# Kernel optimization log

Hardware: AMD Instinct MI355X
Metric: run time of the kernel (lower is better)

Reference implementation:

```python
import jax, jax.numpy as jnp
import numpy as np

B, S, D, H = 2, 2048, 2048, 16
HD = D // H  # 128, head_dim (even, as asserted)
MAX_POS = 2048


def setup_inputs() -> dict:
    key = jax.random.key(0)
    ks = jax.random.split(key, 5)
    x = jax.random.normal(ks[0], (B, S, D), jnp.float32)
    Wq = jax.random.normal(ks[1], (D, D), jnp.float32) * 0.02
    Wk = jax.random.normal(ks[2], (D, D), jnp.float32) * 0.02
    Wv = jax.random.normal(ks[3], (D, D), jnp.float32) * 0.02
    Wo = jax.random.normal(ks[4], (D, D), jnp.float32) * 0.02
    # standard RoPE tables: [MAX_POS, HD]
    inv_freq = 1.0 / (10000.0 ** (jnp.arange(0, HD, 2, dtype=jnp.float32) / HD))
    angles = jnp.arange(MAX_POS, dtype=jnp.float32)[:, None] * inv_freq  # [P, HD/2]
    emb = jnp.concatenate([angles, angles], axis=-1)  # [P, HD]
    cos_freqs = jnp.cos(emb)
    sin_freqs = jnp.sin(emb)
    position_ids = jnp.broadcast_to(jnp.arange(S, dtype=jnp.int32), (B, S))
    return {"x": x, "cos_freqs": cos_freqs, "sin_freqs": sin_freqs,
            "Wq": Wq, "Wk": Wk, "Wv": Wv, "Wo": Wo,
            "position_ids": position_ids}


def _apply_rope(t, cos, sin, position_ids):
    # t: [b, s, h, hd]; cos/sin: [P, hd]; position_ids: [b, s]
    c = cos[position_ids][:, :, None, :]  # [b, s, 1, hd]
    s_ = sin[position_ids][:, :, None, :]
    t1, t2 = jnp.split(t, 2, axis=-1)
    rot = jnp.concatenate([-t2, t1], axis=-1)  # rotate-half
    return t * c + rot * s_


def reference(x, cos_freqs, sin_freqs, Wq, Wk, Wv, Wo, position_ids):
    b, s, d = x.shape
    q = (x @ Wq).reshape(b, s, H, HD)
    k = (x @ Wk).reshape(b, s, H, HD)  # n_kv_heads == n_heads
    v = (x @ Wv).reshape(b, s, H, HD)
    q = _apply_rope(q, cos_freqs, sin_freqs, position_ids)
    k = _apply_rope(k, cos_freqs, sin_freqs, position_ids)
    # [b, h, s, hd]
    q_t = jnp.swapaxes(q, 1, 2)
    k_t = jnp.swapaxes(k, 1, 2)
    v_t = jnp.swapaxes(v, 1, 2)
    scale = 1.0 / jnp.sqrt(jnp.float32(HD))
    scores = jnp.einsum('bhsd,bhtd->bhst', q_t, k_t) * scale  # O(s^2) matrix
    causal = jnp.tril(jnp.ones((s, s), dtype=bool))
    scores = jnp.where(causal[None, None, :, :], scores, -1e9)
    weights = jax.nn.softmax(scores, axis=-1)
    out = jnp.einsum('bhst,bhtd->bhsd', weights, v_t)
    out = jnp.swapaxes(out, 1, 2).reshape(b, s, d)
    out = out @ Wo
    return (out, k, v)  # kv_cache is post-RoPE, pre-transpose as in original
```

## Files before the change

### kernel.cpp

```cpp
#include <hip/hip_runtime.h>
#include <hip/hip_bf16.h>

#define B_ 2
#define S_ 2048
#define D_ 2048
#define H_ 16
#define HD_ 128
#define M_ (B_*S_)
#define BSD ((size_t)B_*S_*D_)

typedef short bf16x8 __attribute__((ext_vector_type(8)));
typedef float floatx4 __attribute__((ext_vector_type(4)));
typedef __hip_bfloat16 bf16;

union cv8 { bf16 h[8]; uint4 u; bf16x8 v; };

__device__ inline cv8 cvt8(const float4 a, const float4 b) {
    cv8 c;
    c.h[0] = __float2bfloat16(a.x); c.h[1] = __float2bfloat16(a.y);
    c.h[2] = __float2bfloat16(a.z); c.h[3] = __float2bfloat16(a.w);
    c.h[4] = __float2bfloat16(b.x); c.h[5] = __float2bfloat16(b.y);
    c.h[6] = __float2bfloat16(b.z); c.h[7] = __float2bfloat16(b.w);
    return c;
}

__device__ __forceinline__ void gld16(const void* g, void* l) {
    __builtin_amdgcn_global_load_lds(
        (const __attribute__((address_space(1))) unsigned int*)g,
        (__attribute__((address_space(3))) unsigned int*)l,
        16, 0, 0);
}

__global__ __launch_bounds__(256) void transpose_w(
    const float* __restrict__ W, bf16* __restrict__ Wt, int N, int K)
{
    __shared__ float T[32][33];
    const int k0 = blockIdx.x * 32, n0 = blockIdx.y * 32;
    const int r = threadIdx.x >> 3, c4 = (threadIdx.x & 7) * 4;
    float4 v = *(const float4*)&W[(size_t)(k0 + r) * N + n0 + c4];
    T[r][c4+0] = v.x; T[r][c4+1] = v.y; T[r][c4+2] = v.z; T[r][c4+3] = v.w;
    __syncthreads();
    union { bf16 h[4]; uint2 u; } o;
    #pragma unroll
    for (int i = 0; i < 4; ++i) o.h[i] = __float2bfloat16(T[c4 + i][r]);
    *(uint2*)&Wt[(size_t)(n0 + r) * K + k0 + c4] = o.u;
}

__global__ __launch_bounds__(256) void transpose_w_s(
    const float* __restrict__ W, bf16* __restrict__ Wt, int N, int K)
{
    __shared__ float T[32][33];
    const int k0 = blockIdx.x * 32, n0 = blockIdx.y * 32;
    const int r = threadIdx.x >> 3, c4 = (threadIdx.x & 7) * 4;
    float4 v = *(const float4*)&W[(size_t)(k0 + r) * N + n0 + c4];
    T[r][c4+0] = v.x; T[r][c4+1] = v.y; T[r][c4+2] = v.z; T[r][c4+3] = v.w;
    __syncthreads();
    union { bf16 h[4]; uint2 u; } o;
    #pragma unroll
    for (int i = 0; i < 4; ++i) o.h[i] = __float2bfloat16(T[c4 + i][r]);
    const int n = n0 + r;
    size_t bo = (size_t)n * (size_t)K * 2 + ((unsigned)((k0 + c4) * 2) ^ ((n & 3) << 4));
    *(uint2*)((char*)Wt + bo) = o.u;
}

__global__ __launch_bounds__(256) void pack_bf16(
    const float* __restrict__ src, bf16* __restrict__ dst)
{
    const size_t i = ((size_t)blockIdx.x * 256 + threadIdx.x) * 8;
    cv8 c = cvt8(*(const float4*)(src + i), *(const float4*)(src + i + 4));
    size_t bo = i * 2;
    bo ^= (size_t)(((bo >> 12) & 3) << 4);
    *(uint4*)((char*)dst + bo) = c.u;
}

__global__ __launch_bounds__(256) void pack_k(
    const float* __restrict__ src, bf16* __restrict__ dst)
{
    const int idx = blockIdx.x * 256 + threadIdx.x;
    const int dg = idx & 15;
    const int s  = (idx >> 4) & (S_ - 1);
    const int h  = (idx >> 15) & (H_ - 1);
    const int b  = idx >> 19;
    const float* sp = src + ((size_t)(b*S_ + s)*H_ + h)*HD_ + dg*8;
    cv8 c = cvt8(*(const float4*)sp, *(const float4*)(sp + 4));
    size_t rowb = ((size_t)(b*H_ + h)*S_ + s) * (size_t)(HD_*2);
    int colb = (dg*16) ^ ((s & 7) << 4);
    *(uint4*)((char*)dst + rowb + colb) = c.u;
}

__global__ __launch_bounds__(256) void pack_vt(
    const float* __restrict__ src, bf16* __restrict__ dst)
{
    __shared__ float T[32][33];
    const int s0 = blockIdx.x * 32;
    const int d0 = blockIdx.y * 32;
    const int bh = blockIdx.z;
    const int b = bh >> 4, h = bh & (H_-1);
    const int r = threadIdx.x >> 3, c4 = (threadIdx.x & 7) * 4;
    float4 v = *(const float4*)&src[((size_t)(b*S_ + s0 + r)*H_ + h)*HD_ + d0 + c4];
    T[r][c4+0] = v.x; T[r][c4+1] = v.y; T[r][c4+2] = v.z; T[r][c4+3] = v.w;
    __syncthreads();
    union { bf16 h4[4]; uint2 u; } o;
    #pragma unroll
    for (int i = 0; i < 4; ++i) o.h4[i] = __float2bfloat16(T[c4 + i][r]);
    const int hd = d0 + r;
    size_t rowb = ((size_t)bh*HD_ + hd) * (size_t)(S_*2);
    size_t colb = (size_t)(s0 + c4) * 2;
    colb = (colb & ~(size_t)127) | (((unsigned)colb & 127u) ^ (unsigned)((hd & 7) << 4));
    *(uint2*)((char*)dst + rowb + colb) = o.u;
}

__global__ __launch_bounds__(256, 3) void gemm_bb2(
    const bf16* __restrict__ A, const bf16* __restrict__ Wt,
    float* __restrict__ C, int M, int N, int K)
{
    __shared__ __align__(16) bf16 As[128][32];
    __shared__ __align__(16) bf16 Bs[128][32];
    const int nwg = (int)(gridDim.x * gridDim.y);
    int id = (int)(blockIdx.y * gridDim.x + blockIdx.x);
    if ((nwg & 7) == 0) id = (id & 7) * (nwg >> 3) + (id >> 3);
    const int m0 = (id % (int)gridDim.x) * 128;
    const int n0 = (id / (int)gridDim.x) * 128;
    const int tid = threadIdx.x, lane = tid & 63, w = tid >> 6;
    const int quad = lane >> 4, l16 = lane & 15;
    const int wrow = (w >> 1) * 64, wcol = (w & 1) * 64;
    const size_t K2 = (size_t)K * 2;

    floatx4 acc[4][4] = {};

    const char* Ab = (const char*)A;
    const char* Bb = (const char*)Wt;
    char* AsB = (char*)&As[0][0];
    char* BsB = (char*)&Bs[0][0];
    const int srow = lane >> 2;
    const int scol = (lane & 3) * 16;

    for (int kt = 0; kt < K; kt += 32) {
        #pragma unroll
        for (int j = 0; j < 2; ++j) {
            const int row = w*32 + j*16 + srow;
            gld16(Ab + (size_t)(m0 + row)*K2 + (size_t)(kt*2) + scol,
                  AsB + w*2048 + j*1024);
            gld16(Bb + (size_t)(n0 + row)*K2 + (size_t)(kt*2) + scol,
                  BsB + w*2048 + j*1024);
        }
        __syncthreads();

        bf16x8 af[4], bfr[4];
        #pragma unroll
        for (int t = 0; t < 4; ++t) {
            const int ra = wrow + t*16 + l16;
            af[t]  = *(const bf16x8*)(AsB + ra*64 + ((quad*16) ^ ((ra & 3) << 4)));
            const int rb = wcol + t*16 + l16;
            bfr[t] = *(const bf16x8*)(BsB + rb*64 + ((quad*16) ^ ((rb & 3) << 4)));
        }
        #pragma unroll
        for (int mt = 0; mt < 4; ++mt)
            #pragma unroll
            for (int nt = 0; nt < 4; ++nt)
                acc[mt][nt] = __builtin_amdgcn_mfma_f32_16x16x32_bf16(
                    af[mt], bfr[nt], acc[mt][nt], 0, 0, 0);
        __syncthreads();
    }

    #pragma unroll
    for (int mt = 0; mt < 4; ++mt)
        #pragma unroll
        for (int nt = 0; nt < 4; ++nt)
            #pragma unroll
            for (int r = 0; r < 4; ++r)
                C[(size_t)(m0 + wrow + mt*16 + quad*4 + r) * N
                  + n0 + wcol + nt*16 + l16] = acc[mt][nt][r];
}

__global__ __launch_bounds__(256) void gemm_xw(
    const float* __restrict__ A, const bf16* __restrict__ Wt,
    float* __restrict__ C, int M, int N, int K)
{
    __shared__ __align__(16) bf16 As[128][40];
    __shared__ __align__(16) bf16 Bs[128][40];
    const int m0 = blockIdx.x * 128, n0 = blockIdx.y * 128;
    const int tid = threadIdx.x, lane = tid & 63, w = tid >> 6;
    const int quad = lane >> 4, l16 = lane & 15;
    const int wrow = (w >> 1) * 64, wcol = (w & 1) * 64;
    floatx4 acc[4][4] = {};
    const int arow = tid >> 2;
    const int acol = (tid & 3) * 8;
    for (int kt = 0; kt < K; kt += 32) {
        #pragma unroll
        for (int p = 0; p < 2; ++p) {
            const int r = p*64 + arow;
            const float* ap = &A[(size_t)(m0 + r) * K + kt + acol];
            cv8 ca = cvt8(*(const float4*)ap, *(const float4*)(ap + 4));
            *(uint4*)&As[r][acol] = ca.u;
            const bf16* bp = &Wt[(size_t)(n0 + r) * K + kt + acol];
            *(uint4*)&Bs[r][acol] = *(const uint4*)bp;
        }
        __syncthreads();
        bf16x8 af[4], bfr[4];
        #pragma unroll
        for (int t = 0; t < 4; ++t) {
            af[t]  = *(const bf16x8*)&As[wrow + t*16 + l16][quad*8];
            bfr[t] = *(const bf16x8*)&Bs[wcol + t*16 + l16][quad*8];
        }
        #pragma unroll
        for (int mt = 0; mt < 4; ++mt)
            #pragma unroll
            for (int nt = 0; nt < 4; ++nt)
                acc[mt][nt] = __builtin_amdgcn_mfma_f32_16x16x32_bf16(
                    af[mt], bfr[nt], acc[mt][nt], 0, 0, 0);
        __syncthreads();
    }
    #pragma unroll
    for (int mt = 0; mt < 4; ++mt)
        #pragma unroll
        for (int nt = 0; nt < 4; ++nt)
            #pragma unroll
            for (int r = 0; r < 4; ++r)
                C[(size_t)(m0 + wrow + mt*16 + quad*4 + r) * N
                  + n0 + wcol + nt*16 + l16] = acc[mt][nt][r];
}

__global__ __launch_bounds__(256) void gemm_f32(
    const float* __restrict__ A, const float* __restrict__ W,
    float* __restrict__ C, int M, int N, int K)
{
    __shared__ __align__(16) bf16 As[64][40];
    __shared__ __align__(16) bf16 Bs[64][40];
    const int m0 = blockIdx.x * 64, n0 = blockIdx.y * 64;
    const int tid = threadIdx.x, lane = tid & 63, w = tid >> 6;
    const int quad = lane >> 4, l16 = lane & 15;
    const int wrow = (w >> 1) * 32, wcol = (w & 1) * 32;
    floatx4 acc[2][2] = {};
    const int ar = tid >> 2, ac = (tid & 3) * 8;
    const int br = tid >> 3, bc = (tid & 7) * 8;
    for (int kt = 0; kt < K; kt += 32) {
        {
            const float* ap = &A[(size_t)(m0 + ar) * K + kt + ac];
            cv8 c = cvt8(*(const float4*)ap, *(const float4*)(ap + 4));
            *(uint4*)&As[ar][ac] = c.u;
        }
        {
            const float* wp = &W[(size_t)(kt + br) * N + n0 + bc];
            cv8 c = cvt8(*(const float4*)wp, *(const float4*)(wp + 4));
            #pragma unroll
            for (int i = 0; i < 8; ++i) Bs[bc + i][br] = c.h[i];
        }
        __syncthreads();
        bf16x8 af[2], bfr[2];
        #pragma unroll
        for (int t = 0; t < 2; ++t) {
            af[t]  = *(const bf16x8*)&As[wrow + t*16 + l16][quad*8];
            bfr[t] = *(const bf16x8*)&Bs[wcol + t*16 + l16][quad*8];
        }
        #pragma unroll
        for (int mt = 0; mt < 2; ++mt)
            #pragma unroll
            for (int nt = 0; nt < 2; ++nt)
                acc[mt][nt] = __builtin_amdgcn_mfma_f32_16x16x32_bf16(
                    af[mt], bfr[nt], acc[mt][nt], 0, 0, 0);
        __syncthreads();
    }
    #pragma unroll
    for (int mt = 0; mt < 2; ++mt)
        #pragma unroll
        for (int nt = 0; nt < 2; ++nt)
            #pragma unroll
            for (int r = 0; r < 4; ++r)
                C[(size_t)(m0 + wrow + mt*16 + quad*4 + r) * N
                  + n0 + wcol + nt*16 + l16] = acc[mt][nt][r];
}

__global__ __launch_bounds__(256) void rope_k(
    float* __restrict__ t,
    const float* __restrict__ cf, const float* __restrict__ sf,
    const int* __restrict__ pos)
{
    const int idx = blockIdx.x * 256 + threadIdx.x;
    const int d  = idx & 63;
    const int h  = (idx >> 6) & (H_-1);
    const int bs = idx >> 10;
    const int p  = pos[bs];
    const float c1 = cf[p*HD_ + d],      s1 = sf[p*HD_ + d];
    const float c2 = cf[p*HD_ + d + 64], s2 = sf[p*HD_ + d + 64];
    const size_t base = (size_t)bs * D_ + h*HD_ + d;
    const float t1 = t[base], t2 = t[base + 64];
    t[base]      = t1*c1 - t2*s1;
    t[base + 64] = t2*c2 + t1*s2;
}

__global__ __launch_bounds__(256) void rope_kernel(
    float* __restrict__ q, float* __restrict__ k,
    const float* __restrict__ cf, const float* __restrict__ sf,
    const int* __restrict__ pos)
{
    const int PAIRS = B_*S_*H_*(HD_/2);
    int idx = blockIdx.x * 256 + threadIdx.x;
    float* t = q;
    if (idx >= PAIRS) { t = k; idx -= PAIRS; }
    const int d  = idx & 63;
    const int h  = (idx >> 6) & (H_-1);
    const int bs = idx >> 10;
    const int p  = pos[bs];
    const float c1 = cf[p*HD_ + d],      s1 = sf[p*HD_ + d];
    const float c2 = cf[p*HD_ + d + 64], s2 = sf[p*HD_ + d + 64];
    const size_t base = (size_t)bs * D_ + h*HD_ + d;
    const float t1 = t[base], t2 = t[base + 64];
    t[base]      = t1*c1 - t2*s1;
    t[base + 64] = t2*c2 + t1*s2;
}

__global__ __launch_bounds__(256, 2) void flash_attn_v4(
    const float* __restrict__ qg, const bf16* __restrict__ kb,
    const bf16* __restrict__ vb, bf16* __restrict__ ob,
    const float* __restrict__ cf, const float* __restrict__ sf,
    const int* __restrict__ pos)
{
    __shared__ __align__(16) bf16 Ks[2][64][128];
    __shared__ __align__(16) bf16 Vt[128][64];
    __shared__ __align__(16) bf16 Ps[4][16][72];

    const int qi = (int)gridDim.x - 1 - (int)blockIdx.x;
    const int q0 = qi * 64;
    const int bh = blockIdx.y;
    const int b = bh >> 4, h = bh & (H_-1);
    const int tid = threadIdx.x, lane = tid & 63, w = tid >> 6;
    const int quad = lane >> 4, l16 = lane & 15;

    const char* kbase = (const char*)(kb + (size_t)bh * S_ * HD_);
    const char* vbase = (const char*)(vb + (size_t)bh * HD_ * S_);
    char* ksd0 = (char*)&Ks[0][0][0];
    char* vtd  = (char*)&Vt[0][0];

    const int klofs = w*4096;
    const int vrow0 = w*32 + (lane >> 3);
    const int vcb   = (lane & 7) * 16;

    #pragma unroll
    for (int j = 0; j < 4; ++j)
        gld16(kbase + klofs + j*1024 + lane*16, ksd0 + klofs + j*1024);

    const int qrow = q0 + w*16 + l16;
    const float* qptr = qg + ((size_t)(b*S_ + qrow))*D_ + h*HD_;
    float rq[4][8];
    #pragma unroll
    for (int c = 0; c < 4; ++c) {
        const float* qp = qptr + c*32 + quad*8;
        *(float4*)&rq[c][0] = *(const float4*)qp;
        *(float4*)&rq[c][4] = *(const float4*)(qp + 4);
    }
    const int p = pos[b*S_ + qrow];
    bf16x8 qf[4];
    #pragma unroll
    for (int c = 0; c < 4; ++c) {
        const float* cp = cf + (size_t)p*HD_ + c*32 + quad*8;
        const float* sp = sf + (size_t)p*HD_ + c*32 + quad*8;
        float cc[8], ss[8];
        *(float4*)&cc[0] = *(const float4*)cp; *(float4*)&cc[4] = *(const float4*)(cp+4);
        *(float4*)&ss[0] = *(const float4*)sp; *(float4*)&ss[4] = *(const float4*)(sp+4);
        cv8 cv;
        #pragma unroll
        for (int j = 0; j < 8; ++j) {
            const float o = (c < 2) ? rq[c][j]*cc[j] - rq[c^2][j]*ss[j]
                                    : rq[c][j]*cc[j] + rq[c^2][j]*ss[j];
            cv.h[j] = __float2bfloat16(o);
        }
        qf[c] = cv.v;
    }

    floatx4 acc_o[8] = {};
    float m_run[4], l_run[4];
    #pragma unroll
    for (int r = 0; r < 4; ++r) { m_run[r] = -30000.0f; l_run[r] = 0.f; }

    __syncthreads();

    for (int kt = 0; kt <= qi; ++kt) {
        const int cur = kt & 1;
        const char* ksb = ksd0 + cur*16384;
        if (kt < qi) {
            const char* src = kbase + (size_t)(kt+1)*16384;
            char* dst = ksd0 + (cur^1)*16384;
            #pragma unroll
            for (int j = 0; j < 4; ++j)
                gld16(src + klofs + j*1024 + lane*16, dst + klofs + j*1024);
        }
        {
            const char* src = vbase + (size_t)kt*128;
            #pragma unroll
            for (int j = 0; j < 4; ++j)
                gld16(src + (size_t)(vrow0 + j*8)*(S_*2) + vcb,
                      vtd + w*4096 + j*1024);
        }

        floatx4 sc[4] = {};
        #pragma unroll
        for (int c = 0; c < 4; ++c) {
            const char* rb = ksb + (c*16 + l16)*256;
            #pragma unroll
            for (int kc = 0; kc < 4; ++kc) {
                bf16x8 kf = *(const bf16x8*)(rb + ((kc*64 + quad*16) ^ ((l16 & 7) << 4)));
                sc[c] = __builtin_amdgcn_mfma_f32_16x16x32_bf16(qf[kc], kf, sc[c], 0, 0, 0);
            }
        }

        const int k0 = kt * 64;
        float pv[4][4], mt_[4];
        #pragma unroll
        for (int r = 0; r < 4; ++r) mt_[r] = -30000.0f;
        #pragma unroll
        for (int c = 0; c < 4; ++c) {
            const int kcol = k0 + c*16 + l16;
            #pragma unroll
            for (int r = 0; r < 4; ++r) {
                const int qr = q0 + w*16 + quad*4 + r;
                float s = sc[c][r] * 0.08838834764831845f;
                if (kcol > qr) s = -30000.0f;
                pv[c][r] = s;
                mt_[r] = fmaxf(mt_[r], s);
            }
        }
        #pragma unroll
        for (int off = 1; off < 16; off <<= 1)
            #pragma unroll
            for (int r = 0; r < 4; ++r)
                mt_[r] = fmaxf(mt_[r], __shfl_xor(mt_[r], off, 64));
        float alpha[4];
        #pragma unroll
        for (int r = 0; r < 4; ++r) {
            float mn = fmaxf(m_run[r], mt_[r]);
            alpha[r] = __expf(m_run[r] - mn);
            m_run[r] = mn;
        }
        #pragma unroll
        for (int c = 0; c < 4; ++c)
            #pragma unroll
            for (int r = 0; r < 4; ++r)
                pv[c][r] = __expf(pv[c][r] - m_run[r]);
        #pragma unroll
        for (int r = 0; r < 4; ++r) {
            float s = pv[0][r] + pv[1][r] + pv[2][r] + pv[3][r];
            #pragma unroll
            for (int off = 1; off < 16; off <<= 1)
                s += __shfl_xor(s, off, 64);
            l_run[r] = l_run[r] * alpha[r] + s;
        }
        #pragma unroll
        for (int c = 0; c < 4; ++c)
            #pragma unroll
            for (int r = 0; r < 4; ++r)
                Ps[w][quad*4 + r][c*16 + l16] = __float2bfloat16(pv[c][r]);
        __syncthreads();

        #pragma unroll
        for (int n = 0; n < 8; ++n)
            #pragma unroll
            for (int r = 0; r < 4; ++r)
                acc_o[n][r] *= alpha[r];
        bf16x8 pf[2];
        #pragma unroll
        for (int kc2 = 0; kc2 < 2; ++kc2)
            pf[kc2] = *(const bf16x8*)&Ps[w][l16][kc2*32 + quad*8];
        #pragma unroll
        for (int n = 0; n < 8; ++n) {
            const char* rb = vtd + (n*16 + l16)*128;
            #pragma unroll
            for (int kc2 = 0; kc2 < 2; ++kc2) {
                bf16x8 vf = *(const bf16x8*)(rb + ((kc2*64 + quad*16) ^ ((l16 & 7) << 4)));
                acc_o[n] = __builtin_amdgcn_mfma_f32_16x16x32_bf16(pf[kc2], vf, acc_o[n], 0, 0, 0);
            }
        }
        __syncthreads();
    }

    float inv[4];
    #pragma unroll
    for (int r = 0; r < 4; ++r) inv[r] = 1.0f / l_run[r];
    #pragma unroll
    for (int n = 0; n < 8; ++n)
        #pragma unroll
        for (int r = 0; r < 4; ++r) {
            const int qr = q0 + w*16 + quad*4 + r;
            size_t bo = ((((size_t)(b*S_ + qr))*D_ + h*HD_ + n*16 + l16) * 2)
                        ^ (size_t)(r << 4);
            *(bf16*)((char*)ob + bo) = __float2bfloat16(acc_o[n][r] * inv[r]);
        }
}

__global__ __launch_bounds__(256) void flash_attn(
    const float* qg, const float* __restrict__ kg,
    const float* __restrict__ vg, float* og)
{
    __shared__ __align__(16) bf16 Ks[64][136];
    __shared__ __align__(16) bf16 Vt[128][72];
    __shared__ __align__(16) bf16 Ps[4][16][72];

    const int qi = (int)gridDim.x - 1 - (int)blockIdx.x;
    const int q0 = qi * 64;
    const int bh = blockIdx.y;
    const int b = bh >> 4, h = bh & (H_-1);
    const int tid = threadIdx.x, lane = tid & 63, w = tid >> 6;
    const int quad = lane >> 4, l16 = lane & 15;

    const int qrow = q0 + w*16 + l16;
    const float* qptr = qg + ((size_t)(b*S_ + qrow)*H_ + h)*HD_;
    bf16x8 qf[4];
    #pragma unroll
    for (int c = 0; c < 4; ++c) {
        const float* qp = qptr + c*32 + quad*8;
        cv8 cv = cvt8(*(const float4*)qp, *(const float4*)(qp + 4));
        qf[c] = cv.v;
    }

    floatx4 acc_o[8] = {};
    float m_run[4], l_run[4];
    #pragma unroll
    for (int r = 0; r < 4; ++r) { m_run[r] = -30000.0f; l_run[r] = 0.f; }

    const int ksr = tid >> 2, kscg = (tid & 3) * 32;
    const int vk2 = (tid & 31) * 2, vf8 = (tid >> 5) * 8;

    for (int kt = 0; kt <= qi; ++kt) {
        const int k0 = kt * 64;
        {
            const float* kp = kg + ((size_t)(b*S_ + k0 + ksr)*H_ + h)*HD_ + kscg;
            #pragma unroll
            for (int j = 0; j < 4; ++j) {
                cv8 c = cvt8(*(const float4*)(kp + j*8), *(const float4*)(kp + j*8 + 4));
                *(uint4*)&Ks[ksr][kscg + j*8] = c.u;
            }
        }
        {
            #pragma unroll
            for (int pq = 0; pq < 2; ++pq) {
                const int f = vf8 + pq*64;
                const float* v0p = vg + ((size_t)(b*S_ + k0 + vk2)*H_ + h)*HD_ + f;
                const float* v1p = v0p + D_;
                cv8 c0 = cvt8(*(const float4*)v0p, *(const float4*)(v0p + 4));
                cv8 c1 = cvt8(*(const float4*)v1p, *(const float4*)(v1p + 4));
                #pragma unroll
                for (int i = 0; i < 8; ++i) {
                    union { bf16 h2[2]; unsigned u; } pk;
                    pk.h2[0] = c0.h[i]; pk.h2[1] = c1.h[i];
                    *(unsigned*)&Vt[f + i][vk2] = pk.u;
                }
            }
        }
        __syncthreads();

        floatx4 sc[4] = {};
        #pragma unroll
        for (int c = 0; c < 4; ++c)
            #pragma unroll
            for (int kc = 0; kc < 4; ++kc) {
                bf16x8 kf = *(const bf16x8*)&Ks[c*16 + l16][kc*32 + quad*8];
                sc[c] = __builtin_amdgcn_mfma_f32_16x16x32_bf16(qf[kc], kf, sc[c], 0, 0, 0);
            }

        float pv[4][4], mt_[4];
        #pragma unroll
        for (int r = 0; r < 4; ++r) mt_[r] = -30000.0f;
        #pragma unroll
        for (int c = 0; c < 4; ++c) {
            const int kcol = k0 + c*16 + l16;
            #pragma unroll
            for (int r = 0; r < 4; ++r) {
                const int qr = q0 + w*16 + quad*4 + r;
                float s = sc[c][r] * 0.08838834764831845f;
                if (kcol > qr) s = -30000.0f;
                pv[c][r] = s;
                mt_[r] = fmaxf(mt_[r], s);
            }
        }
        #pragma unroll
        for (int off = 1; off < 16; off <<= 1)
            #pragma unroll
            for (int r = 0; r < 4; ++r)
                mt_[r] = fmaxf(mt_[r], __shfl_xor(mt_[r], off, 64));
        float alpha[4];
        #pragma unroll
        for (int r = 0; r < 4; ++r) {
            float mn = fmaxf(m_run[r], mt_[r]);
            alpha[r] = __expf(m_run[r] - mn);
            m_run[r] = mn;
        }
        #pragma unroll
        for (int c = 0; c < 4; ++c)
            #pragma unroll
            for (int r = 0; r < 4; ++r)
                pv[c][r] = __expf(pv[c][r] - m_run[r]);
        #pragma unroll
        for (int r = 0; r < 4; ++r) {
            float s = pv[0][r] + pv[1][r] + pv[2][r] + pv[3][r];
            #pragma unroll
            for (int off = 1; off < 16; off <<= 1)
                s += __shfl_xor(s, off, 64);
            l_run[r] = l_run[r] * alpha[r] + s;
        }
        #pragma unroll
        for (int c = 0; c < 4; ++c)
            #pragma unroll
            for (int r = 0; r < 4; ++r)
                Ps[w][quad*4 + r][c*16 + l16] = __float2bfloat16(pv[c][r]);
        __syncthreads();

        #pragma unroll
        for (int n = 0; n < 8; ++n)
            #pragma unroll
            for (int r = 0; r < 4; ++r)
                acc_o[n][r] *= alpha[r];
        bf16x8 pf[2];
        #pragma unroll
        for (int kc2 = 0; kc2 < 2; ++kc2)
            pf[kc2] = *(const bf16x8*)&Ps[w][l16][kc2*32 + quad*8];
        #pragma unroll
        for (int n = 0; n < 8; ++n)
            #pragma unroll
            for (int kc2 = 0; kc2 < 2; ++kc2) {
                bf16x8 vf = *(const bf16x8*)&Vt[n*16 + l16][kc2*32 + quad*8];
                acc_o[n] = __builtin_amdgcn_mfma_f32_16x16x32_bf16(pf[kc2], vf, acc_o[n], 0, 0, 0);
            }
        __syncthreads();
    }

    #pragma unroll
    for (int n = 0; n < 8; ++n)
        #pragma unroll
        for (int r = 0; r < 4; ++r) {
            const int qr = q0 + w*16 + quad*4 + r;
            og[((size_t)(b*S_ + qr))*D_ + h*HD_ + n*16 + l16] = acc_o[n][r] / l_run[r];
        }
}

extern "C" void kernel_launch(void* const* d_in, const int* in_sizes, int n_in,
                              void* d_out, int out_size, void* d_ws, size_t ws_size,
                              hipStream_t stream) {
    const float* x  = (const float*)d_in[0];
    const float* cf = (const float*)d_in[1];
    const float* sf = (const float*)d_in[2];
    const float* Wq = (const float*)d_in[3];
    const float* Wk = (const float*)d_in[4];
    const float* Wv = (const float*)d_in[5];
    const float* Wo = (const float*)d_in[6];
    const int*  pos = (const int*)d_in[7];

    float* out  = (float*)d_out;
    float* kout = out + BSD;
    float* vout = out + 2*BSD;

    const size_t WT_BYTES = (size_t)D_ * D_ * sizeof(bf16);
    const size_t TB_BYTES = BSD * sizeof(bf16);
    const size_t NEED_V4  = WT_BYTES + 4 * TB_BYTES;
    const bool big = ws_size >= WT_BYTES + (size_t)128 * D_ * sizeof(float);

    if (ws_size >= NEED_V4) {
        bf16* wt  = (bf16*)d_ws;
        bf16* xb  = wt + (size_t)D_ * D_;
        bf16* kbb = xb + BSD;
        bf16* vbb = kbb + BSD;
        bf16* obb = vbb + BSD;

        dim3 tg(D_/32, D_/32), gg(M_/128, D_/128);
        pack_bf16<<<(int)(BSD/8/256), 256, 0, stream>>>(x, xb);
        transpose_w_s<<<tg, 256, 0, stream>>>(Wq, wt, D_, D_);
        gemm_bb2<<<gg, 256, 0, stream>>>(xb, wt, out,  M_, D_, D_);
        transpose_w_s<<<tg, 256, 0, stream>>>(Wk, wt, D_, D_);
        gemm_bb2<<<gg, 256, 0, stream>>>(xb, wt, kout, M_, D_, D_);
        transpose_w_s<<<tg, 256, 0, stream>>>(Wv, wt, D_, D_);
        gemm_bb2<<<gg, 256, 0, stream>>>(xb, wt, vout, M_, D_, D_);
        rope_k<<<(B_*S_*H_*(HD_/2))/256, 256, 0, stream>>>(kout, cf, sf, pos);
        pack_k<<<(int)(BSD/8/256), 256, 0, stream>>>(kout, kbb);
        pack_vt<<<dim3(S_/32, HD_/32, B_*H_), 256, 0, stream>>>(vout, vbb);
        flash_attn_v4<<<dim3(S_/64, B_*H_), 256, 0, stream>>>(out, kbb, vbb, obb,
                                                              cf, sf, pos);
        transpose_w_s<<<tg, 256, 0, stream>>>(Wo, wt, D_, D_);
        gemm_bb2<<<gg, 256, 0, stream>>>(obb, wt, out, M_, D_, D_);
    } else if (big) {
        bf16*  wt  = (bf16*)d_ws;
        float* cws = (float*)((char*)d_ws + WT_BYTES);
        const size_t crem = ws_size - WT_BYTES;
        dim3 tg(D_/32, D_/32), gg(M_/128, D_/128);
        transpose_w<<<tg, 256, 0, stream>>>(Wq, wt, D_, D_);
        gemm_xw<<<gg, 256, 0, stream>>>(x, wt, out,  M_, D_, D_);
        transpose_w<<<tg, 256, 0, stream>>>(Wk, wt, D_, D_);
        gemm_xw<<<gg, 256, 0, stream>>>(x, wt, kout, M_, D_, D_);
        transpose_w<<<tg, 256, 0, stream>>>(Wv, wt, D_, D_);
        gemm_xw<<<gg, 256, 0, stream>>>(x, wt, vout, M_, D_, D_);
        rope_kernel<<<(2*B_*S_*H_*(HD_/2))/256, 256, 0, stream>>>(out, kout, cf, sf, pos);
        flash_attn<<<dim3(S_/64, B_*H_), 256, 0, stream>>>(out, kout, vout, out);
        transpose_w<<<tg, 256, 0, stream>>>(Wo, wt, D_, D_);
        int R = 128;
        while (R < M_ && (size_t)(2*R) * D_ * sizeof(float) <= crem) R *= 2;
        for (int m0 = 0; m0 < M_; m0 += R) {
            gemm_xw<<<dim3(R/128, D_/128), 256, 0, stream>>>(out + (size_t)m0*D_, wt, cws, R, D_, D_);
            hipMemcpyAsync(out + (size_t)m0*D_, cws, (size_t)R*D_*sizeof(float),
                           hipMemcpyDeviceToDevice, stream);
        }
    } else {
        float* wsb = (float*)d_ws;
        dim3 gg(M_/64, D_/64);
        gemm_f32<<<gg, 256, 0, stream>>>(x, Wq, out,  M_, D_, D_);
        gemm_f32<<<gg, 256, 0, stream>>>(x, Wk, kout, M_, D_, D_);
        gemm_f32<<<gg, 256, 0, stream>>>(x, Wv, vout, M_, D_, D_);
        rope_kernel<<<(2*B_*S_*H_*(HD_/2))/256, 256, 0, stream>>>(out, kout, cf, sf, pos);
        flash_attn<<<dim3(S_/64, B_*H_), 256, 0, stream>>>(out, kout, vout, out);
        int R = 64;
        while (R < M_ && (size_t)(2*R) * D_ * sizeof(float) <= ws_size) R *= 2;
        if ((size_t)R * D_ * sizeof(float) > ws_size) R = 64;
        for (int m0 = 0; m0 < M_; m0 += R) {
            gemm_f32<<<dim3(R/64, D_/64), 256, 0, stream>>>(out + (size_t)m0*D_, Wo, wsb, R, D_, D_);
            hipMemcpyAsync(out + (size_t)m0*D_, wsb, (size_t)R*D_*sizeof(float),
                           hipMemcpyDeviceToDevice, stream);
        }
    }
}
```

Baseline: 587.2 us.

## Double-buffer V in flash attention and fuse K rope with bf16 packing

Flash attention now double-buffers V tiles in LDS alongside K, prefetching the next tile before computing. It preloads K/V fragments into registers and wraps the MFMA bursts with s_setprio. The softmax uses exp2 with the log2e factor folded into the scale, and the per-iteration barrier after the per-warp P write is dropped. The separate rope and K-packing kernels are merged into one vectorized kernel, saving a full pass over K. The cost is more LDS per block and higher register pressure, which could hurt occupancy.

```diff
diff --git a/kernel.cpp b/kernel.cpp
--- a/kernel.cpp
+++ b/kernel.cpp
@@ -1,5 +1,6 @@
 #include <hip/hip_runtime.h>
 #include <hip/hip_bf16.h>
+#include <math.h>
 
 #define B_ 2
 #define S_ 2048
@@ -73,19 +74,49 @@
     *(uint4*)((char*)dst + bo) = c.u;
 }
 
-__global__ __launch_bounds__(256) void pack_k(
-    const float* __restrict__ src, bf16* __restrict__ dst)
+__global__ __launch_bounds__(256) void rope_pack_k(
+    float* __restrict__ k, bf16* __restrict__ kbb,
+    const float* __restrict__ cf, const float* __restrict__ sf,
+    const int* __restrict__ pos)
 {
     const int idx = blockIdx.x * 256 + threadIdx.x;
-    const int dg = idx & 15;
-    const int s  = (idx >> 4) & (S_ - 1);
-    const int h  = (idx >> 15) & (H_ - 1);
-    const int b  = idx >> 19;
-    const float* sp = src + ((size_t)(b*S_ + s)*H_ + h)*HD_ + dg*8;
-    cv8 c = cvt8(*(const float4*)sp, *(const float4*)(sp + 4));
-    size_t rowb = ((size_t)(b*H_ + h)*S_ + s) * (size_t)(HD_*2);
-    int colb = (dg*16) ^ ((s & 7) << 4);
-    *(uint4*)((char*)dst + rowb + colb) = c.u;
+    const int dg = idx & 7;
+    const int h  = (idx >> 3) & (H_-1);
+    const int bs = idx >> 7;
+    const int s  = bs & (S_-1);
+    const int b  = bs >> 11;
+    const int p  = pos[bs];
+    const size_t base = (size_t)bs * D_ + h*HD_ + dg*8;
+    float lo[8], hi[8], c1[8], s1[8], c2[8], s2[8];
+    *(float4*)&lo[0] = *(const float4*)&k[base];
+    *(float4*)&lo[4] = *(const float4*)&k[base + 4];
+    *(float4*)&hi[0] = *(const float4*)&k[base + 64];
+    *(float4*)&hi[4] = *(const float4*)&k[base + 68];
+    const float* cp = cf + (size_t)p*HD_ + dg*8;
+    const float* sp = sf + (size_t)p*HD_ + dg*8;
+    *(float4*)&c1[0] = *(const float4*)cp;        *(float4*)&c1[4] = *(const float4*)(cp + 4);
+    *(float4*)&s1[0] = *(const float4*)sp;        *(float4*)&s1[4] = *(const float4*)(sp + 4);
+    *(float4*)&c2[0] = *(const float4*)(cp + 64); *(float4*)&c2[4] = *(const float4*)(cp + 68);
+    *(float4*)&s2[0] = *(const float4*)(sp + 64); *(float4*)&s2[4] = *(const float4*)(sp + 68);
+    float nl[8], nh[8];
+    #pragma unroll
+    for (int j = 0; j < 8; ++j) {
+        nl[j] = lo[j]*c1[j] - hi[j]*s1[j];
+        nh[j] = hi[j]*c2[j] + lo[j]*s2[j];
+    }
+    *(float4*)&k[base]      = *(float4*)&nl[0];
+    *(float4*)&k[base + 4]  = *(float4*)&nl[4];
+    *(float4*)&k[base + 64] = *(float4*)&nh[0];
+    *(float4*)&k[base + 68] = *(float4*)&nh[4];
+    cv8 clo, chi;
+    #pragma unroll
+    for (int j = 0; j < 8; ++j) {
+        clo.h[j] = __float2bfloat16(nl[j]);
+        chi.h[j] = __float2bfloat16(nh[j]);
+    }
+    const size_t rowb = ((size_t)(b*H_ + h)*S_ + s) * (size_t)(HD_*2);
+    *(uint4*)((char*)kbb + rowb + ((dg*16)       ^ ((s & 7) << 4))) = clo.u;
+    *(uint4*)((char*)kbb + rowb + (((dg+8)*16)   ^ ((s & 7) << 4))) = chi.u;
 }
 
 __global__ __launch_bounds__(256) void pack_vt(
@@ -271,24 +302,6 @@
                   + n0 + wcol + nt*16 + l16] = acc[mt][nt][r];
 }
 
-__global__ __launch_bounds__(256) void rope_k(
-    float* __restrict__ t,
-    const float* __restrict__ cf, const float* __restrict__ sf,
-    const int* __restrict__ pos)
-{
-    const int idx = blockIdx.x * 256 + threadIdx.x;
-    const int d  = idx & 63;
-    const int h  = (idx >> 6) & (H_-1);
-    const int bs = idx >> 10;
-    const int p  = pos[bs];
-    const float c1 = cf[p*HD_ + d],      s1 = sf[p*HD_ + d];
-    const float c2 = cf[p*HD_ + d + 64], s2 = sf[p*HD_ + d + 64];
-    const size_t base = (size_t)bs * D_ + h*HD_ + d;
-    const float t1 = t[base], t2 = t[base + 64];
-    t[base]      = t1*c1 - t2*s1;
-    t[base + 64] = t2*c2 + t1*s2;
-}
-
 __global__ __launch_bounds__(256) void rope_kernel(
     float* __restrict__ q, float* __restrict__ k,
     const float* __restrict__ cf, const float* __restrict__ sf,
@@ -310,14 +323,14 @@
     t[base + 64] = t2*c2 + t1*s2;
 }
 
-__global__ __launch_bounds__(256, 2) void flash_attn_v4(
+__global__ __launch_bounds__(256, 2) void flash_attn_v5(
     const float* __restrict__ qg, const bf16* __restrict__ kb,
     const bf16* __restrict__ vb, bf16* __restrict__ ob,
     const float* __restrict__ cf, const float* __restrict__ sf,
     const int* __restrict__ pos)
 {
     __shared__ __align__(16) bf16 Ks[2][64][128];
-    __shared__ __align__(16) bf16 Vt[128][64];
+    __shared__ __align__(16) bf16 Vt[2][128][64];
     __shared__ __align__(16) bf16 Ps[4][16][72];
 
     const int qi = (int)gridDim.x - 1 - (int)blockIdx.x;
@@ -329,8 +342,8 @@
 
     const char* kbase = (const char*)(kb + (size_t)bh * S_ * HD_);
     const char* vbase = (const char*)(vb + (size_t)bh * HD_ * S_);
-    char* ksd0 = (char*)&Ks[0][0][0];
-    char* vtd  = (char*)&Vt[0][0];
+    char* ksd = (char*)&Ks[0][0][0];
+    char* vtd = (char*)&Vt[0][0][0];
 
     const int klofs = w*4096;
     const int vrow0 = w*32 + (lane >> 3);
@@ -338,7 +351,10 @@
 
     #pragma unroll
     for (int j = 0; j < 4; ++j)
-        gld16(kbase + klofs + j*1024 + lane*16, ksd0 + klofs + j*1024);
+        gld16(kbase + klofs + j*1024 + lane*16, ksd + klofs + j*1024);
+    #pragma unroll
+    for (int j = 0; j < 4; ++j)
+        gld16(vbase + (size_t)(vrow0 + j*8)*(S_*2) + vcb, vtd + w*4096 + j*1024);
 
     const int qrow = q0 + w*16 + l16;
     const float* qptr = qg + ((size_t)(b*S_ + qrow))*D_ + h*HD_;
@@ -373,36 +389,45 @@
     #pragma unroll
     for (int r = 0; r < 4; ++r) { m_run[r] = -30000.0f; l_run[r] = 0.f; }
 
+    const float SCL2 = 0.08838834764831845f * 1.4426950408889634f;
+
     __syncthreads();
 
     for (int kt = 0; kt <= qi; ++kt) {
         const int cur = kt & 1;
-        const char* ksb = ksd0 + cur*16384;
+        const char* ksb = ksd + cur*16384;
+        const char* vtb = vtd + cur*16384;
+
+        bf16x8 kf[4][4];
+        #pragma unroll
+        for (int c = 0; c < 4; ++c)
+            #pragma unroll
+            for (int kc = 0; kc < 4; ++kc)
+                kf[c][kc] = *(const bf16x8*)(ksb + (c*16 + l16)*256
+                              + ((kc*64 + quad*16) ^ ((l16 & 7) << 4)));
+
         if (kt < qi) {
-            const char* src = kbase + (size_t)(kt+1)*16384;
-            char* dst = ksd0 + (cur^1)*16384;
+            const char* ksrc = kbase + (size_t)(kt+1)*16384;
+            char* kdst = ksd + (cur^1)*16384;
             #pragma unroll
             for (int j = 0; j < 4; ++j)
-                gld16(src + klofs + j*1024 + lane*16, dst + klofs + j*1024);
-        }
-        {
-            const char* src = vbase + (size_t)kt*128;
+                gld16(ksrc + klofs + j*1024 + lane*16, kdst + klofs + j*1024);
+            const char* vsrc = vbase + (size_t)(kt+1)*128;
+            char* vdst = vtd + (cur^1)*16384;
             #pragma unroll
             for (int j = 0; j < 4; ++j)
-                gld16(src + (size_t)(vrow0 + j*8)*(S_*2) + vcb,
-                      vtd + w*4096 + j*1024);
+                gld16(vsrc + (size_t)(vrow0 + j*8)*(S_*2) + vcb,
+                      vdst + w*4096 + j*1024);
         }
 
         floatx4 sc[4] = {};
-        #pragma unroll
-        for (int c = 0; c < 4; ++c) {
-            const char* rb = ksb + (c*16 + l16)*256;
-            #pragma unroll
-            for (int kc = 0; kc < 4; ++kc) {
-                bf16x8 kf = *(const bf16x8*)(rb + ((kc*64 + quad*16) ^ ((l16 & 7) << 4)));
-                sc[c] = __builtin_amdgcn_mfma_f32_16x16x32_bf16(qf[kc], kf, sc[c], 0, 0, 0);
-            }
-        }
+        __builtin_amdgcn_s_setprio(1);
+        #pragma unroll
+        for (int c = 0; c < 4; ++c)
+            #pragma unroll
+            for (int kc = 0; kc < 4; ++kc)
+                sc[c] = __builtin_amdgcn_mfma_f32_16x16x32_bf16(qf[kc], kf[c][kc], sc[c], 0, 0, 0);
+        __builtin_amdgcn_s_setprio(0);
 
         const int k0 = kt * 64;
         float pv[4][4], mt_[4];
@@ -414,7 +439,7 @@
             #pragma unroll
             for (int r = 0; r < 4; ++r) {
                 const int qr = q0 + w*16 + quad*4 + r;
-                float s = sc[c][r] * 0.08838834764831845f;
+                float s = sc[c][r] * SCL2;
                 if (kcol > qr) s = -30000.0f;
                 pv[c][r] = s;
                 mt_[r] = fmaxf(mt_[r], s);
@@ -429,14 +454,14 @@
         #pragma unroll
         for (int r = 0; r < 4; ++r) {
             float mn = fmaxf(m_run[r], mt_[r]);
-            alpha[r] = __expf(m_run[r] - mn);
+            alpha[r] = exp2f(m_run[r] - mn);
             m_run[r] = mn;
         }
         #pragma unroll
         for (int c = 0; c < 4; ++c)
             #pragma unroll
             for (int r = 0; r < 4; ++r)
-                pv[c][r] = __expf(pv[c][r] - m_run[r]);
+                pv[c][r] = exp2f(pv[c][r] - m_run[r]);
         #pragma unroll
         for (int r = 0; r < 4; ++r) {
             float s = pv[0][r] + pv[1][r] + pv[2][r] + pv[3][r];
@@ -450,7 +475,6 @@
             #pragma unroll
             for (int r = 0; r < 4; ++r)
                 Ps[w][quad*4 + r][c*16 + l16] = __float2bfloat16(pv[c][r]);
-        __syncthreads();
 
         #pragma unroll
         for (int n = 0; n < 8; ++n)
@@ -461,15 +485,21 @@
         #pragma unroll
         for (int kc2 = 0; kc2 < 2; ++kc2)
             pf[kc2] = *(const bf16x8*)&Ps[w][l16][kc2*32 + quad*8];
-        #pragma unroll
-        for (int n = 0; n < 8; ++n) {
-            const char* rb = vtd + (n*16 + l16)*128;
-            #pragma unroll
-            for (int kc2 = 0; kc2 < 2; ++kc2) {
-                bf16x8 vf = *(const bf16x8*)(rb + ((kc2*64 + quad*16) ^ ((l16 & 7) << 4)));
-                acc_o[n] = __builtin_amdgcn_mfma_f32_16x16x32_bf16(pf[kc2], vf, acc_o[n], 0, 0, 0);
-            }
-        }
+        bf16x8 vf[8][2];
+        #pragma unroll
+        for (int n = 0; n < 8; ++n)
+            #pragma unroll
+            for (int kc2 = 0; kc2 < 2; ++kc2)
+                vf[n][kc2] = *(const bf16x8*)(vtb + (n*16 + l16)*128
+                               + ((kc2*64 + quad*16) ^ ((l16 & 7) << 4)));
+        __builtin_amdgcn_s_setprio(1);
+        #pragma unroll
+        for (int n = 0; n < 8; ++n)
+            #pragma unroll
+            for (int kc2 = 0; kc2 < 2; ++kc2)
+                acc_o[n] = __builtin_amdgcn_mfma_f32_16x16x32_bf16(pf[kc2], vf[n][kc2], acc_o[n], 0, 0, 0);
+        __builtin_amdgcn_s_setprio(0);
+
         __syncthreads();
     }
 
@@ -650,10 +680,10 @@
 
     const size_t WT_BYTES = (size_t)D_ * D_ * sizeof(bf16);
     const size_t TB_BYTES = BSD * sizeof(bf16);
-    const size_t NEED_V4  = WT_BYTES + 4 * TB_BYTES;
+    const size_t NEED_V5  = WT_BYTES + 4 * TB_BYTES;
     const bool big = ws_size >= WT_BYTES + (size_t)128 * D_ * sizeof(float);
 
-    if (ws_size >= NEED_V4) {
+    if (ws_size >= NEED_V5) {
         bf16* wt  = (bf16*)d_ws;
         bf16* xb  = wt + (size_t)D_ * D_;
         bf16* kbb = xb + BSD;
@@ -668,10 +698,9 @@
         gemm_bb2<<<gg, 256, 0, stream>>>(xb, wt, kout, M_, D_, D_);
         transpose_w_s<<<tg, 256, 0, stream>>>(Wv, wt, D_, D_);
         gemm_bb2<<<gg, 256, 0, stream>>>(xb, wt, vout, M_, D_, D_);
-        rope_k<<<(B_*S_*H_*(HD_/2))/256, 256, 0, stream>>>(kout, cf, sf, pos);
-        pack_k<<<(int)(BSD/8/256), 256, 0, stream>>>(kout, kbb);
+        rope_pack_k<<<(B_*S_*H_*8)/256, 256, 0, stream>>>(kout, kbb, cf, sf, pos);
         pack_vt<<<dim3(S_/32, HD_/32, B_*H_), 256, 0, stream>>>(vout, vbb);
-        flash_attn_v4<<<dim3(S_/64, B_*H_), 256, 0, stream>>>(out, kbb, vbb, obb,
+        flash_attn_v5<<<dim3(S_/64, B_*H_), 256, 0, stream>>>(out, kbb, vbb, obb,
                                                               cf, sf, pos);
         transpose_w_s<<<tg, 256, 0, stream>>>(Wo, wt, D_, D_);
         gemm_bb2<<<gg, 256, 0, stream>>>(obb, wt, out, M_, D_, D_);
```

New measurement: 592.6 us. No clear change (+0.9%).
